# Optimization experiments

Measured on AMD Instinct MI355X. Metric: run time of the kernel, lower is better.

The kernel has to match this reference:

```python
import jax, jax.numpy as jnp
import numpy as np
from jax import lax

B, U, D = 16, 2048, 512


def setup_inputs() -> dict:
    key = jax.random.key(0)
    ks = jax.random.split(key, 6)
    xs = jax.random.normal(ks[0], (B, U, D), dtype=jnp.float32)
    xlens = jax.random.randint(ks[1], (B,), U // 2, U + 1).astype(jnp.int32)
    ylens = jax.random.randint(ks[2], (B,), 128, 257).astype(jnp.int32)
    # Conv1d(D, D, kernel_size=3, padding=1): weight [O, I, K], bias [O]
    conv_w = jax.random.normal(ks[3], (D, D, 3), dtype=jnp.float32) * (1.0 / np.sqrt(3 * D))
    conv_b = jnp.zeros((D,), dtype=jnp.float32)
    # Linear(D, 1)
    lin_w = jax.random.normal(ks[4], (1, D), dtype=jnp.float32) * (1.0 / np.sqrt(D))
    lin_b = jnp.zeros((1,), dtype=jnp.float32)
    return {"xs": xs, "xlens": xlens, "ylens": ylens,
            "conv_w": conv_w, "conv_b": conv_b, "lin_w": lin_w, "lin_b": lin_b}


def _forward(xs, xlens, ylens, conv_w, conv_b, lin_w, lin_b, u_max):
    # alpha gate: conv1d -> relu -> linear -> sigmoid
    h = lax.conv_general_dilated(xs.transpose(0, 2, 1), conv_w, (1,), ((1, 1),),
                                 dimension_numbers=("NCH", "OIH", "NCH"))
    h = jax.nn.relu(h + conv_b[None, :, None])          # [B, D, U]
    alpha = jax.nn.sigmoid(jnp.einsum("bdu,od->bu", h, lin_w) + lin_b[0])  # [B, U]
    # zero padded positions (positions >= xlen)
    pos = jnp.arange(U)[None, :]
    alpha = jnp.where(pos >= xlens[:, None], 0.0, alpha)
    sum_alpha = alpha.sum(-1)                            # [B]
    beta = sum_alpha / ylens.astype(sum_alpha.dtype) - 1e-4  # [B]

    def step(carry, inp):
        prev_alpha, prev_state = carry                   # [B], [B, D]
        cur_alpha, cur_state = inp                       # [B], [B, D]
        new_alpha = prev_alpha + cur_alpha
        fired = new_alpha >= beta                        # [B]
        left = (beta - prev_alpha)[:, None]
        right = (new_alpha - beta)[:, None]
        integ = prev_state + left * cur_state            # integrated state at fire
        next_alpha = jnp.where(fired, right[:, 0], new_alpha)
        next_state = jnp.where(fired[:, None], right * cur_state, integ)
        next_fired = jnp.where(fired[:, None], integ, jnp.zeros_like(integ))
        return (next_alpha, next_state), next_fired

    init = (jnp.zeros((B,), xs.dtype), jnp.zeros((B, D), xs.dtype))
    _, fired_seq = lax.scan(step, init, (alpha.T, xs.transpose(1, 0, 2)))
    fired_state = fired_seq.transpose(1, 0, 2)           # [B, U, D]

    # stable-move fired frames to the front of each batch row
    marks = jnp.abs(fired_state).sum(-1) != 0.0          # [B, U] bool
    order = jnp.argsort(~marks, axis=1, stable=True)     # fired (False-key) first
    cif_output = jnp.take_along_axis(fired_state, order[:, :, None], axis=1)
    h_cif = cif_output[:, :u_max, :]
    return h_cif, sum_alpha


def reference(xs, xlens, ylens, conv_w, conv_b, lin_w, lin_b):
    u_max = int(jnp.max(ylens))
    return _forward(xs, xlens, ylens, conv_w, conv_b, lin_w, lin_b, u_max)
```

## Files before the change

kernel.cpp:

```cpp
#include <hip/hip_runtime.h>
#include <cstddef>
#include <cstdint>

#define Bb 16
#define Uu 2048
#define Dd 512
#define BU (Bb*Uu)

typedef short bf16x8 __attribute__((ext_vector_type(8)));
typedef float f32x4 __attribute__((ext_vector_type(4)));

#define ROW_BYTES 144
#define A_BYTES 18720
#define B_SLICE 18432
#define B_BASE (2*A_BYTES)
#define STEP_BYTES (512*ROW_BYTES)
#define SMEM_BYTES (B_BASE + 2*B_SLICE)

#define WAITVM(N) asm volatile("s_waitcnt vmcnt(" #N ")" ::: "memory")
#define WAITLGKM0 asm volatile("s_waitcnt lgkmcnt(0)" ::: "memory")

__device__ __forceinline__ unsigned short f2bf(float x){
  unsigned int u = __float_as_uint(x);
  u += 0x7fff + ((u >> 16) & 1);
  return (unsigned short)(u >> 16);
}
__device__ __forceinline__ float bf2f(unsigned short b){
  return __uint_as_float(((unsigned int)b) << 16);
}

union U16x8 { unsigned short s[8]; uint4 v; };

__device__ __forceinline__ void split2(float x, unsigned short& h, unsigned short& m){
  h = f2bf(x);
  float r1 = x - bf2f(h);
  m = f2bf(r1);
}

__global__ __launch_bounds__(256) void pack_b_kernel(const float* __restrict__ conv_w,
                                                     char* __restrict__ Bpack){
  int idx = blockIdx.x * 256 + threadIdx.x;
  int n = idx >> 6, cg = idx & 63;
  int chunk = cg >> 2, sub = cg & 3, c0 = cg << 3;
  const float* src = conv_w + (size_t)n * (Dd * 3) + (size_t)c0 * 3;
  float w[24];
  #pragma unroll
  for (int j = 0; j < 24; ++j) w[j] = src[j];
  #pragma unroll
  for (int tap = 0; tap < 3; ++tap){
    U16x8 H, M;
    #pragma unroll
    for (int j = 0; j < 8; ++j) split2(w[j * 3 + tap], H.s[j], M.s[j]);
    char* dst = Bpack + (size_t)(chunk * 3 + tap) * STEP_BYTES + n * ROW_BYTES + sub * 16;
    *(uint4*)dst = H.v;
    *(uint4*)(dst + 64) = M.v;
  }
}

__device__ __forceinline__ void stage_A_direct(char* abuf, const float* __restrict__ xsb,
                                               int u0, int c0, int tid){
  #pragma unroll
  for (int it = 0; it < 2; ++it){
    if (it == 0 || tid < 8){
      int t = tid + it * 512;
      int r = t >> 2, cg = t & 3;
      int uu = u0 - 1 + r;
      float x[8];
      if (uu >= 0 && uu < Uu){
        const float* p = xsb + (size_t)uu * Dd + c0 + cg * 8;
        float4 a = *(const float4*)p;
        float4 b = *(const float4*)(p + 4);
        x[0]=a.x; x[1]=a.y; x[2]=a.z; x[3]=a.w; x[4]=b.x; x[5]=b.y; x[6]=b.z; x[7]=b.w;
      } else {
        #pragma unroll
        for (int j = 0; j < 8; ++j) x[j] = 0.f;
      }
      U16x8 H, M;
      #pragma unroll
      for (int j = 0; j < 8; ++j) split2(x[j], H.s[j], M.s[j]);
      char* dst = abuf + r * ROW_BYTES + cg * 16;
      *(uint4*)(dst)      = H.v;
      *(uint4*)(dst + 64) = M.v;
    }
  }
}

__device__ __forceinline__ void gll16(const char* g, char* l){
  __builtin_amdgcn_global_load_lds(
      (const __attribute__((address_space(1))) unsigned int*)g,
      (__attribute__((address_space(3))) unsigned int*)l, 16, 0, 0);
}

__device__ __forceinline__ void stage_slice(char* ldsB, const char* __restrict__ src,
                                            int lane, int wv){
  const char* g = src + wv * 1024 + lane * 16;
  char* l = ldsB + wv * 1024;
  gll16(g, l);
  gll16(g + 8192, l + 8192);
  if (wv < 2) gll16(g + 16384, l + 16384);
}

__device__ __forceinline__ bf16x8 ldfrag(const char* p){
  return __builtin_bit_cast(bf16x8, *(const uint4*)p);
}

__global__ __launch_bounds__(512, 4) void conv_mfma_full_kernel(
    const float* __restrict__ xs, const char* __restrict__ Bpack,
    const float* __restrict__ conv_b, const float* __restrict__ lin_w,
    float* __restrict__ partial)
{
  __shared__ __align__(16) char smem[SMEM_BYTES];
  const int tid = threadIdx.x;
  const int lane = tid & 63, wv = tid >> 6;
  const int wm = wv & 3;
  const int wn = wv >> 2;
  const int cs = blockIdx.x >> 8;
  const int bt = blockIdx.x & 255;
  const int b = bt >> 4, ut = bt & 15;
  const int u0 = ut * 128;
  const float* xsb = xs + (size_t)b * Uu * Dd;
  const int li = lane & 15, lg = lane >> 4;

  f32x4 acc[2][4];
  #pragma unroll
  for (int m = 0; m < 2; ++m)
    #pragma unroll
    for (int n = 0; n < 4; ++n){
      f32x4 z = {0.f, 0.f, 0.f, 0.f};
      acc[m][n] = z;
    }

  stage_A_direct(smem, xsb, u0, 0, tid);
  stage_slice(smem + B_BASE, Bpack + cs * B_SLICE, lane, wv);
  __syncthreads();

  for (int chunk = 0; chunk < 16; ++chunk){
    const bool more = (chunk < 15);
    const char* aC = smem + (chunk & 1) * A_BYTES;
    char* aN = smem + ((chunk & 1) ^ 1) * A_BYTES;
    #pragma unroll
    for (int tap = 0; tap < 3; ++tap){
      const int p = chunk * 3 + tap;
      const int bbuf = p & 1;
      const bool apf_now = (tap == 2) && more;

      float4 apf0, apf1, apf2, apf3;
      int ar_ = 0, acg_ = 0, r2_ = 0, cg2_ = 0;
      if (apf_now){
        int c0n = (chunk + 1) * 32;
        ar_ = tid >> 2; acg_ = tid & 3;
        int uu = u0 - 1 + ar_;
        if (uu >= 0 && uu < Uu){
          const float* pp = xsb + (size_t)uu * Dd + c0n + acg_ * 8;
          apf0 = *(const float4*)pp;
          apf1 = *(const float4*)(pp + 4);
        } else {
          apf0 = make_float4(0.f,0.f,0.f,0.f); apf1 = apf0;
        }
        int t2 = 512 + wv;
        r2_ = t2 >> 2; cg2_ = t2 & 3;
        apf2 = make_float4(0.f,0.f,0.f,0.f); apf3 = apf2;
        if (lane == 0){
          int uu2 = u0 - 1 + r2_;
          if (uu2 >= 0 && uu2 < Uu){
            const float* p2 = xsb + (size_t)uu2 * Dd + c0n + cg2_ * 8;
            apf2 = *(const float4*)p2;
            apf3 = *(const float4*)(p2 + 4);
          }
        }
        __builtin_amdgcn_sched_barrier(0);
      }

      if (p < 47)
        stage_slice(smem + B_BASE + (bbuf ^ 1) * B_SLICE,
                    Bpack + (size_t)(p + 1) * STEP_BYTES + cs * B_SLICE, lane, wv);

      if (p == 47)            { WAITVM(0); }
      else if (apf_now)       { if (wv < 2) WAITVM(7); else WAITVM(6); }
      else                    { if (wv < 2) WAITVM(3); else WAITVM(2); }
      __builtin_amdgcn_sched_barrier(0);

      bf16x8 a[2][2];
      #pragma unroll
      for (int m = 0; m < 2; ++m){
        const char* ar = aC + (size_t)(wm * 32 + m * 16 + li + tap) * ROW_BYTES + lg * 16;
        a[m][0] = ldfrag(ar);
        a[m][1] = ldfrag(ar + 64);
      }

      __builtin_amdgcn_s_setprio(1);
      const char* bbase = smem + B_BASE + bbuf * B_SLICE;
      #pragma unroll
      for (int n = 0; n < 4; ++n){
        const char* br = bbase + (size_t)(wn * 64 + n * 16 + li) * ROW_BYTES + lg * 16;
        bf16x8 bh = ldfrag(br);
        bf16x8 bm = ldfrag(br + 64);
        #pragma unroll
        for (int m = 0; m < 2; ++m){
          acc[m][n] = __builtin_amdgcn_mfma_f32_16x16x32_bf16(a[m][0], bh, acc[m][n], 0, 0, 0);
          acc[m][n] = __builtin_amdgcn_mfma_f32_16x16x32_bf16(a[m][1], bh, acc[m][n], 0, 0, 0);
          acc[m][n] = __builtin_amdgcn_mfma_f32_16x16x32_bf16(a[m][0], bm, acc[m][n], 0, 0, 0);
          acc[m][n] = __builtin_amdgcn_mfma_f32_16x16x32_bf16(a[m][1], bm, acc[m][n], 0, 0, 0);
        }
      }
      __builtin_amdgcn_s_setprio(0);

      if (apf_now){
        if (wv < 2) { WAITVM(3); } else { WAITVM(2); }
        __builtin_amdgcn_sched_barrier(0);
        U16x8 H, M;
        float x[8];
        x[0]=apf0.x; x[1]=apf0.y; x[2]=apf0.z; x[3]=apf0.w;
        x[4]=apf1.x; x[5]=apf1.y; x[6]=apf1.z; x[7]=apf1.w;
        #pragma unroll
        for (int jj = 0; jj < 8; ++jj) split2(x[jj], H.s[jj], M.s[jj]);
        char* dst = aN + ar_ * ROW_BYTES + acg_ * 16;
        *(uint4*)(dst)      = H.v;
        *(uint4*)(dst + 64) = M.v;
        if (lane == 0){
          float y[8];
          y[0]=apf2.x; y[1]=apf2.y; y[2]=apf2.z; y[3]=apf2.w;
          y[4]=apf3.x; y[5]=apf3.y; y[6]=apf3.z; y[7]=apf3.w;
          #pragma unroll
          for (int jj = 0; jj < 8; ++jj) split2(y[jj], H.s[jj], M.s[jj]);
          char* dst2 = aN + r2_ * ROW_BYTES + cg2_ * 16;
          *(uint4*)(dst2)      = H.v;
          *(uint4*)(dst2 + 64) = M.v;
        }
        WAITLGKM0;
        __builtin_amdgcn_sched_barrier(0);
      }
      __builtin_amdgcn_s_barrier();
    }
  }

  __syncthreads();
  float* pbuf = (float*)smem;
  #pragma unroll
  for (int m = 0; m < 2; ++m){
    float s0 = 0.f, s1 = 0.f, s2 = 0.f, s3 = 0.f;
    #pragma unroll
    for (int n = 0; n < 4; ++n){
      int col = cs * 128 + wn * 64 + n * 16 + li;
      float cb = conv_b[col], lw = lin_w[col];
      f32x4 v = acc[m][n];
      float h;
      h = v[0] + cb; h = h > 0.f ? h : 0.f; s0 += h * lw;
      h = v[1] + cb; h = h > 0.f ? h : 0.f; s1 += h * lw;
      h = v[2] + cb; h = h > 0.f ? h : 0.f; s2 += h * lw;
      h = v[3] + cb; h = h > 0.f ? h : 0.f; s3 += h * lw;
    }
    #pragma unroll
    for (int msk = 1; msk < 16; msk <<= 1){
      s0 += __shfl_xor(s0, msk); s1 += __shfl_xor(s1, msk);
      s2 += __shfl_xor(s2, msk); s3 += __shfl_xor(s3, msk);
    }
    if (li == 0){
      int fr = wm * 32 + m * 16 + lg * 4;
      pbuf[(fr + 0) * 2 + wn] = s0;
      pbuf[(fr + 1) * 2 + wn] = s1;
      pbuf[(fr + 2) * 2 + wn] = s2;
      pbuf[(fr + 3) * 2 + wn] = s3;
    }
  }
  __syncthreads();
  if (tid < 128){
    float pv = pbuf[tid * 2] + pbuf[tid * 2 + 1];
    partial[(size_t)cs * BU + (size_t)b * Uu + u0 + tid] = pv;
  }
}

__global__ __launch_bounds__(64) void scan_kernel(
    const float* __restrict__ partial, const float* __restrict__ lin_b,
    const int* __restrict__ xlens, const int* __restrict__ ylens,
    float* __restrict__ wA, float* __restrict__ wB,
    int* __restrict__ fire_pos, int* __restrict__ nf,
    float* __restrict__ out_sum)
{
  __shared__ float salpha[Uu];
  int b = blockIdx.x;
  int lane = threadIdx.x;
  int xl = xlens[b];
  float lb = lin_b[0];

  float sum = 0.f;
  for (int u0 = 0; u0 < Uu; u0 += 64){
    int u = u0 + lane;
    size_t ix = (size_t)b * Uu + u;
    float v = lb + partial[ix] + partial[BU + ix] + partial[2 * BU + ix] + partial[3 * BU + ix];
    float a = 1.f / (1.f + expf(-v));
    if (u >= xl) a = 0.f;
    salpha[u] = a;
    sum += a;
  }
  #pragma unroll
  for (int m = 1; m < 64; m <<= 1) sum += __shfl_xor(sum, m);
  float sa = sum;
  float beta = sa / (float)ylens[b] - 1e-4f;
  if (lane == 0) out_sum[b] = sa;

  float prev = 0.f;
  int cnt = 0;
  for (int u0 = 0; u0 < Uu; u0 += 64) {
    if (u0 >= xl) break;
    float val = salpha[u0 + lane];
    float mywa = 0.f, mywb = 0.f;
    #pragma unroll
    for (int i = 0; i < 64; ++i) {
      float a_cur = __builtin_bit_cast(float,
          __builtin_amdgcn_readlane(__builtin_bit_cast(int, val), i));
      float nw = prev + a_cur;
      float left = beta - prev;
      float right = nw - beta;
      bool fired = nw >= beta;
      if (lane == i) { mywa = left; mywb = right; }
      if (fired) {
        if (lane == 0) fire_pos[(b << 11) + cnt] = u0 + i;
        ++cnt;
      }
      prev = fired ? right : nw;
    }
    wA[(size_t)b * Uu + u0 + lane] = mywa;
    wB[(size_t)b * Uu + u0 + lane] = mywb;
  }
  if (lane == 0) nf[b] = cnt;
}

__global__ __launch_bounds__(512) void gather_kernel(
    const float* __restrict__ xs, const float* __restrict__ wA, const float* __restrict__ wB,
    const int* __restrict__ fire_pos, const int* __restrict__ nf,
    float* __restrict__ out, int umax)
{
  int t = blockIdx.x, b = blockIdx.y;
  int tid = threadIdx.x;
  float* o = out + ((size_t)b * umax + t) * Dd;
  int n = nf[b];
  if (t >= n) { o[tid] = 0.f; return; }
  int start = (t == 0) ? 0 : fire_pos[(b << 11) + t - 1];
  int end = fire_pos[(b << 11) + t];
  const float* xb = xs + (size_t)b * Uu * Dd;
  float acc = 0.f;
  for (int u = start; u <= end; ++u) {
    float w = (t > 0 && u == start) ? wB[(size_t)b * Uu + u] : wA[(size_t)b * Uu + u];
    acc += w * xb[(size_t)u * Dd + tid];
  }
  o[tid] = acc;
}

extern "C" void kernel_launch(void* const* d_in, const int* in_sizes, int n_in,
                              void* d_out, int out_size, void* d_ws, size_t ws_size,
                              hipStream_t stream) {
  const float* xs     = (const float*)d_in[0];
  const int*   xlens  = (const int*)d_in[1];
  const int*   ylens  = (const int*)d_in[2];
  const float* conv_w = (const float*)d_in[3];
  const float* conv_b = (const float*)d_in[4];
  const float* lin_w  = (const float*)d_in[5];
  const float* lin_b  = (const float*)d_in[6];
  float* out = (float*)d_out;
  int umax = (out_size - Bb) / (Bb * Dd);

  char* ws = (char*)d_ws;
  char*  Bpack    = ws;
  float* partial  = (float*)(ws + 48 * (size_t)STEP_BYTES);
  float* wAv      = partial + 4 * BU;
  float* wBv      = wAv + BU;
  int*   fire_pos = (int*)(wBv + BU);
  int*   nf       = (int*)(fire_pos + BU);

  pack_b_kernel<<<(512 * 64) / 256, 256, 0, stream>>>(conv_w, Bpack);
  conv_mfma_full_kernel<<<1024, 512, 0, stream>>>(xs, Bpack, conv_b, lin_w, partial);
  scan_kernel<<<Bb, 64, 0, stream>>>(partial, lin_b, xlens, ylens, wAv, wBv, fire_pos, nf,
                                     out + (size_t)Bb * umax * Dd);
  if (umax > 0)
    gather_kernel<<<dim3(umax, Bb), 512, 0, stream>>>(xs, wAv, wBv, fire_pos, nf, out, umax);
}
```

Before: 272.4 us.

## Halve conv block to 4 waves with 64x64 per-wave MFMA tiles

Shrinks the conv MFMA block from 8 to 4 waves (256 threads) while keeping the same 128x128 output tile. Each wave now computes a 64x64 sub-tile (4x4 accumulators) instead of 32x64. This doubles A-fragment reuse per B load and halves LDS fragment reads per MFMA. The staging loops, vmcnt wait counts and epilogue indexing are rewritten to match. In exchange it raises register pressure and cuts waves per CU, which may hide latency less well.

```diff
diff --git a/kernel.cpp b/kernel.cpp
--- a/kernel.cpp
+++ b/kernel.cpp
@@ -60,9 +60,9 @@
 __device__ __forceinline__ void stage_A_direct(char* abuf, const float* __restrict__ xsb,
                                                int u0, int c0, int tid){
   #pragma unroll
-  for (int it = 0; it < 2; ++it){
-    if (it == 0 || tid < 8){
-      int t = tid + it * 512;
+  for (int it = 0; it < 3; ++it){
+    if (it < 2 || tid < 8){
+      int t = (it < 2) ? (tid + it * 256) : (512 + tid);
       int r = t >> 2, cg = t & 3;
       int uu = u0 - 1 + r;
       float x[8];
@@ -96,7 +96,9 @@
   const char* g = src + wv * 1024 + lane * 16;
   char* l = ldsB + wv * 1024;
   gll16(g, l);
-  gll16(g + 8192, l + 8192);
+  gll16(g + 4096,  l + 4096);
+  gll16(g + 8192,  l + 8192);
+  gll16(g + 12288, l + 12288);
   if (wv < 2) gll16(g + 16384, l + 16384);
 }
 
@@ -104,7 +106,7 @@
   return __builtin_bit_cast(bf16x8, *(const uint4*)p);
 }
 
-__global__ __launch_bounds__(512, 4) void conv_mfma_full_kernel(
+__global__ __launch_bounds__(256, 2) void conv_mfma_full_kernel(
     const float* __restrict__ xs, const char* __restrict__ Bpack,
     const float* __restrict__ conv_b, const float* __restrict__ lin_w,
     float* __restrict__ partial)
@@ -112,8 +114,8 @@
   __shared__ __align__(16) char smem[SMEM_BYTES];
   const int tid = threadIdx.x;
   const int lane = tid & 63, wv = tid >> 6;
-  const int wm = wv & 3;
-  const int wn = wv >> 2;
+  const int wm = wv >> 1;
+  const int wn = wv & 1;
   const int cs = blockIdx.x >> 8;
   const int bt = blockIdx.x & 255;
   const int b = bt >> 4, ut = bt & 15;
@@ -121,9 +123,9 @@
   const float* xsb = xs + (size_t)b * Uu * Dd;
   const int li = lane & 15, lg = lane >> 4;
 
-  f32x4 acc[2][4];
-  #pragma unroll
-  for (int m = 0; m < 2; ++m)
+  f32x4 acc[4][4];
+  #pragma unroll
+  for (int m = 0; m < 4; ++m)
     #pragma unroll
     for (int n = 0; n < 4; ++n){
       f32x4 z = {0.f, 0.f, 0.f, 0.f};
@@ -144,28 +146,31 @@
       const int bbuf = p & 1;
       const bool apf_now = (tap == 2) && more;
 
-      float4 apf0, apf1, apf2, apf3;
-      int ar_ = 0, acg_ = 0, r2_ = 0, cg2_ = 0;
+      float4 pa0, pa1, pb0, pb1, pe0, pe1;
+      int rA = 0, cgA = 0;
       if (apf_now){
+        const float4 z4 = make_float4(0.f,0.f,0.f,0.f);
+        pa0 = z4; pa1 = z4; pe0 = z4; pe1 = z4;
         int c0n = (chunk + 1) * 32;
-        ar_ = tid >> 2; acg_ = tid & 3;
-        int uu = u0 - 1 + ar_;
-        if (uu >= 0 && uu < Uu){
-          const float* pp = xsb + (size_t)uu * Dd + c0n + acg_ * 8;
-          apf0 = *(const float4*)pp;
-          apf1 = *(const float4*)(pp + 4);
-        } else {
-          apf0 = make_float4(0.f,0.f,0.f,0.f); apf1 = apf0;
+        rA = tid >> 2; cgA = tid & 3;
+        int uuA = u0 - 1 + rA;
+        if (uuA >= 0){
+          const float* pp = xsb + (size_t)uuA * Dd + c0n + cgA * 8;
+          pa0 = *(const float4*)pp;
+          pa1 = *(const float4*)(pp + 4);
         }
-        int t2 = 512 + wv;
-        r2_ = t2 >> 2; cg2_ = t2 & 3;
-        apf2 = make_float4(0.f,0.f,0.f,0.f); apf3 = apf2;
-        if (lane == 0){
-          int uu2 = u0 - 1 + r2_;
-          if (uu2 >= 0 && uu2 < Uu){
-            const float* p2 = xsb + (size_t)uu2 * Dd + c0n + cg2_ * 8;
-            apf2 = *(const float4*)p2;
-            apf3 = *(const float4*)(p2 + 4);
+        {
+          const float* pp = xsb + (size_t)(u0 + 63 + rA) * Dd + c0n + cgA * 8;
+          pb0 = *(const float4*)pp;
+          pb1 = *(const float4*)(pp + 4);
+        }
+        if (wv == 0){
+          int rE = 128 + (lane >> 2);
+          int uuE = u0 - 1 + rE;
+          if (lane < 8 && uuE < Uu){
+            const float* pp = xsb + (size_t)uuE * Dd + c0n + (lane & 3) * 8;
+            pe0 = *(const float4*)pp;
+            pe1 = *(const float4*)(pp + 4);
           }
         }
         __builtin_amdgcn_sched_barrier(0);
@@ -176,14 +181,14 @@
                     Bpack + (size_t)(p + 1) * STEP_BYTES + cs * B_SLICE, lane, wv);
 
       if (p == 47)            { WAITVM(0); }
-      else if (apf_now)       { if (wv < 2) WAITVM(7); else WAITVM(6); }
-      else                    { if (wv < 2) WAITVM(3); else WAITVM(2); }
+      else if (apf_now)       { if (wv == 0) WAITVM(11); else if (wv == 1) WAITVM(9); else WAITVM(8); }
+      else                    { if (wv < 2) WAITVM(5); else WAITVM(4); }
       __builtin_amdgcn_sched_barrier(0);
 
-      bf16x8 a[2][2];
+      bf16x8 a[4][2];
       #pragma unroll
-      for (int m = 0; m < 2; ++m){
-        const char* ar = aC + (size_t)(wm * 32 + m * 16 + li + tap) * ROW_BYTES + lg * 16;
+      for (int m = 0; m < 4; ++m){
+        const char* ar = aC + (size_t)(wm * 64 + m * 16 + li + tap) * ROW_BYTES + lg * 16;
         a[m][0] = ldfrag(ar);
         a[m][1] = ldfrag(ar + 64);
       }
@@ -196,36 +201,46 @@
         bf16x8 bh = ldfrag(br);
         bf16x8 bm = ldfrag(br + 64);
         #pragma unroll
-        for (int m = 0; m < 2; ++m){
-          acc[m][n] = __builtin_amdgcn_mfma_f32_16x16x32_bf16(a[m][0], bh, acc[m][n], 0, 0, 0);
-          acc[m][n] = __builtin_amdgcn_mfma_f32_16x16x32_bf16(a[m][1], bh, acc[m][n], 0, 0, 0);
-          acc[m][n] = __builtin_amdgcn_mfma_f32_16x16x32_bf16(a[m][0], bm, acc[m][n], 0, 0, 0);
-          acc[m][n] = __builtin_amdgcn_mfma_f32_16x16x32_bf16(a[m][1], bm, acc[m][n], 0, 0, 0);
-        }
+        for (int m = 0; m < 4; ++m) acc[m][n] = __builtin_amdgcn_mfma_f32_16x16x32_bf16(a[m][0], bh, acc[m][n], 0, 0, 0);
+        #pragma unroll
+        for (int m = 0; m < 4; ++m) acc[m][n] = __builtin_amdgcn_mfma_f32_16x16x32_bf16(a[m][1], bh, acc[m][n], 0, 0, 0);
+        #pragma unroll
+        for (int m = 0; m < 4; ++m) acc[m][n] = __builtin_amdgcn_mfma_f32_16x16x32_bf16(a[m][0], bm, acc[m][n], 0, 0, 0);
+        #pragma unroll
+        for (int m = 0; m < 4; ++m) acc[m][n] = __builtin_amdgcn_mfma_f32_16x16x32_bf16(a[m][1], bm, acc[m][n], 0, 0, 0);
       }
       __builtin_amdgcn_s_setprio(0);
 
       if (apf_now){
-        if (wv < 2) { WAITVM(3); } else { WAITVM(2); }
+        if (wv < 2) { WAITVM(5); } else { WAITVM(4); }
         __builtin_amdgcn_sched_barrier(0);
         U16x8 H, M;
         float x[8];
-        x[0]=apf0.x; x[1]=apf0.y; x[2]=apf0.z; x[3]=apf0.w;
-        x[4]=apf1.x; x[5]=apf1.y; x[6]=apf1.z; x[7]=apf1.w;
+        x[0]=pa0.x; x[1]=pa0.y; x[2]=pa0.z; x[3]=pa0.w;
+        x[4]=pa1.x; x[5]=pa1.y; x[6]=pa1.z; x[7]=pa1.w;
         #pragma unroll
         for (int jj = 0; jj < 8; ++jj) split2(x[jj], H.s[jj], M.s[jj]);
-        char* dst = aN + ar_ * ROW_BYTES + acg_ * 16;
+        char* dst = aN + rA * ROW_BYTES + cgA * 16;
         *(uint4*)(dst)      = H.v;
         *(uint4*)(dst + 64) = M.v;
-        if (lane == 0){
-          float y[8];
-          y[0]=apf2.x; y[1]=apf2.y; y[2]=apf2.z; y[3]=apf2.w;
-          y[4]=apf3.x; y[5]=apf3.y; y[6]=apf3.z; y[7]=apf3.w;
-          #pragma unroll
-          for (int jj = 0; jj < 8; ++jj) split2(y[jj], H.s[jj], M.s[jj]);
-          char* dst2 = aN + r2_ * ROW_BYTES + cg2_ * 16;
-          *(uint4*)(dst2)      = H.v;
-          *(uint4*)(dst2 + 64) = M.v;
+        x[0]=pb0.x; x[1]=pb0.y; x[2]=pb0.z; x[3]=pb0.w;
+        x[4]=pb1.x; x[5]=pb1.y; x[6]=pb1.z; x[7]=pb1.w;
+        #pragma unroll
+        for (int jj = 0; jj < 8; ++jj) split2(x[jj], H.s[jj], M.s[jj]);
+        char* dst2 = aN + (64 + rA) * ROW_BYTES + cgA * 16;
+        *(uint4*)(dst2)      = H.v;
+        *(uint4*)(dst2 + 64) = M.v;
+        if (wv == 0){
+          if (lane < 8){
+            float y[8];
+            y[0]=pe0.x; y[1]=pe0.y; y[2]=pe0.z; y[3]=pe0.w;
+            y[4]=pe1.x; y[5]=pe1.y; y[6]=pe1.z; y[7]=pe1.w;
+            #pragma unroll
+            for (int jj = 0; jj < 8; ++jj) split2(y[jj], H.s[jj], M.s[jj]);
+            char* dst3 = aN + (128 + (lane >> 2)) * ROW_BYTES + (lane & 3) * 16;
+            *(uint4*)(dst3)      = H.v;
+            *(uint4*)(dst3 + 64) = M.v;
+          }
         }
         WAITLGKM0;
         __builtin_amdgcn_sched_barrier(0);
@@ -237,7 +252,7 @@
   __syncthreads();
   float* pbuf = (float*)smem;
   #pragma unroll
-  for (int m = 0; m < 2; ++m){
+  for (int m = 0; m < 4; ++m){
     float s0 = 0.f, s1 = 0.f, s2 = 0.f, s3 = 0.f;
     #pragma unroll
     for (int n = 0; n < 4; ++n){
@@ -256,7 +271,7 @@
       s2 += __shfl_xor(s2, msk); s3 += __shfl_xor(s3, msk);
     }
     if (li == 0){
-      int fr = wm * 32 + m * 16 + lg * 4;
+      int fr = wm * 64 + m * 16 + lg * 4;
       pbuf[(fr + 0) * 2 + wn] = s0;
       pbuf[(fr + 1) * 2 + wn] = s1;
       pbuf[(fr + 2) * 2 + wn] = s2;
@@ -369,7 +384,7 @@
   int*   nf       = (int*)(fire_pos + BU);
 
   pack_b_kernel<<<(512 * 64) / 256, 256, 0, stream>>>(conv_w, Bpack);
-  conv_mfma_full_kernel<<<1024, 512, 0, stream>>>(xs, Bpack, conv_b, lin_w, partial);
+  conv_mfma_full_kernel<<<1024, 256, 0, stream>>>(xs, Bpack, conv_b, lin_w, partial);
   scan_kernel<<<Bb, 64, 0, stream>>>(partial, lin_b, xlens, ylens, wAv, wBv, fire_pos, nf,
                                      out + (size_t)Bb * umax * Dd);
   if (umax > 0)
```

After: 271.3 us. About the same (-0.4%).
